# Kernel tuning notes

Measured on AMD Instinct MI355X. Metric: run time of the kernel, lower is better.

## Reference

```python
import jax, jax.numpy as jnp
import numpy as np

B, C_LIDAR, C_CAM = 2, 384, 80
H = W = 180
HW = H * W
HID, NCLS, P, NH, DFF, L, NMS_K = 128, 10, 200, 8, 256, 2, 3


def conv2d(x, w, b):
    y = jax.lax.conv_general_dilated(x, w, (1, 1), 'SAME', dimension_numbers=('NCHW', 'OIHW', 'NCHW'))
    return y + b[None, :, None, None]


def conv1d3(x, w, b):
    y = jax.lax.conv_general_dilated(x, w, (1,), 'SAME', dimension_numbers=('NCH', 'OIH', 'NCH'))
    return y + b[None, :, None]


def layer_norm(x, g, b, eps=1e-5):
    mu = jnp.mean(x, -1, keepdims=True)
    var = jnp.mean((x - mu) ** 2, -1, keepdims=True)
    return (x - mu) * jax.lax.rsqrt(var + eps) * g + b


def mha(q, k, v, wqkv, bqkv, wo, bo):
    Bq, Nq, C = q.shape
    dh = C // NH
    qh = (q @ wqkv[0].T + bqkv[0]).reshape(Bq, Nq, NH, dh)
    kh = (k @ wqkv[1].T + bqkv[1]).reshape(k.shape[0], -1, NH, dh)
    vh = (v @ wqkv[2].T + bqkv[2]).reshape(v.shape[0], -1, NH, dh)
    att = jax.nn.softmax(jnp.einsum('bqhd,bkhd->bhqk', qh, kh) * np.float32(1.0 / np.sqrt(dh)), axis=-1)
    out = jnp.einsum('bhqk,bkhd->bqhd', att, vh).reshape(Bq, Nq, C)
    return out @ wo.T + bo


def posembed(pos, w1, b1, g, bt, w2, b2):
    # Conv1d(2->C,k1) + BN(inference) + ReLU + Conv1d(C->C,k1); pos [B,N,2] -> [B,N,C]
    x = pos @ w1.T + b1
    x = jax.nn.relu(x * g + bt)
    return x @ w2.T + b2


def reference(lidar, cam, shared_w, shared_b, fused_w, fused_b, hm_w1, hm_b1, hm_g, hm_beta, hm_w2, hm_b2, ce_w, ce_b, pe_w1, pe_b1, pe_g, pe_beta, pe_w2, pe_b2, attn_wqkv, attn_bqkv, attn_wo, attn_bo, ln_g, ln_b, ffn_w1, ffn_b1, ffn_w2, ffn_b2, hc_w1, hc_b1, hc_g, hc_beta, hc_w2, hc_b2, hh_w1, hh_b1, hh_g, hh_beta, hh_w2, hh_b2):
    cam_feat = conv2d(cam, fused_w, fused_b)            # [B,HID,H,W]
    lidar_feat = conv2d(lidar, shared_w, shared_b)      # [B,HID,H,W]
    lidar_flat = lidar_feat.reshape(B, HID, HW)
    key_flat = cam_feat.reshape(B, HID, HW).transpose(0, 2, 1)   # [B,HW,HID]
    # heatmap head: ConvModule(conv+BN+ReLU) then conv -> classes
    h = jax.nn.relu(conv2d(lidar_feat, hm_w1, hm_b1) * hm_g[None, :, None, None] + hm_beta[None, :, None, None])
    dense_heatmap = conv2d(h, hm_w2, hm_b2)             # [B,NCLS,H,W]
    heatmap = jax.nn.sigmoid(jax.lax.stop_gradient(dense_heatmap))
    # max-pool local-max NMS
    pad = NMS_K // 2
    inner = jax.lax.reduce_window(heatmap, -jnp.inf, jax.lax.max, (1, 1, NMS_K, NMS_K), (1, 1, 1, 1), 'VALID')
    local_max = jnp.zeros_like(heatmap).at[:, :, pad:-pad, pad:-pad].set(inner)
    # nuScenes: classes 8,9 use kernel-size-1 pooling (identity)
    local_max = local_max.at[:, 8].set(heatmap[:, 8]).at[:, 9].set(heatmap[:, 9])
    heatmap = heatmap * (heatmap == local_max)
    # top-k proposals over flattened class*HW scores (== descending argsort[:P])
    _, top = jax.lax.top_k(heatmap.reshape(B, -1), P)
    top_cls = top // HW
    top_idx = top % HW
    qf = jnp.take_along_axis(lidar_flat, top_idx[:, None, :], axis=2)   # [B,HID,P]
    one_hot = jax.nn.one_hot(top_cls, NCLS, dtype=qf.dtype)             # [B,P,NCLS]
    qf = qf + (one_hot @ ce_w.T + ce_b).transpose(0, 2, 1)
    # BEV position grid (x/y cell centers, ij order matching HW flattening)
    gx = jnp.arange(H, dtype=qf.dtype) + 0.5
    gy = jnp.arange(W, dtype=qf.dtype) + 0.5
    bev = jnp.stack(jnp.meshgrid(gx, gy, indexing='ij'), -1).reshape(HW, 2)
    qpos = bev[top_idx]                                  # [B,P,2]
    x = qf.transpose(0, 2, 1)                            # [B,P,HID]
    for i in range(L):
        qpe = posembed(qpos, pe_w1[i, 0], pe_b1[i, 0], pe_g[i, 0], pe_beta[i, 0], pe_w2[i, 0], pe_b2[i, 0])
        kpe = posembed(bev[None], pe_w1[i, 1], pe_b1[i, 1], pe_g[i, 1], pe_beta[i, 1], pe_w2[i, 1], pe_b2[i, 1])
        k = key_flat + kpe
        sa = mha(x + qpe, x + qpe, x + qpe, attn_wqkv[i, 0], attn_bqkv[i, 0], attn_wo[i, 0], attn_bo[i, 0])
        x = layer_norm(x + sa, ln_g[i, 0], ln_b[i, 0])
        ca = mha(x + qpe, k, k, attn_wqkv[i, 1], attn_bqkv[i, 1], attn_wo[i, 1], attn_bo[i, 1])
        x = layer_norm(x + ca, ln_g[i, 1], ln_b[i, 1])
        f = jax.nn.relu(x @ ffn_w1[i].T + ffn_b1[i]) @ ffn_w2[i].T + ffn_b2[i]
        x = layer_norm(x + f, ln_g[i, 2], ln_b[i, 2])
        xc = x.transpose(0, 2, 1)                        # [B,HID,P]
        yc = jax.nn.relu(conv1d3(xc, hc_w1[i], hc_b1[i]) * hc_g[i][None, :, None] + hc_beta[i][None, :, None])
        center = conv1d3(yc, hc_w2[i], hc_b2[i]) + qpos.transpose(0, 2, 1)
        yh = jax.nn.relu(conv1d3(xc, hh_w1[i], hh_b1[i]) * hh_g[i][None, :, None] + hh_beta[i][None, :, None])
        hm_pred = conv1d3(yh, hh_w2[i], hh_b2[i])
        qpos = jax.lax.stop_gradient(center).transpose(0, 2, 1)   # .detach().clone().permute
    return jnp.concatenate([center, hm_pred], axis=1)   # [B, 2+NCLS, P]


def _n(key, i, shape, s=0.02):
    return s * jax.random.normal(jax.random.fold_in(key, i), shape, dtype=jnp.float32)


def setup_inputs():
    key = jax.random.key(0)
    z, o = jnp.zeros, jnp.ones
    return dict(
        lidar=jax.random.normal(jax.random.fold_in(key, 100), (B, C_LIDAR, H, W), dtype=jnp.float32),
        cam=jax.random.normal(jax.random.fold_in(key, 101), (B, C_CAM, H, W), dtype=jnp.float32),
        shared_w=_n(key, 0, (HID, C_LIDAR, 3, 3)), shared_b=z((HID,)),
        fused_w=_n(key, 1, (HID, C_CAM, 3, 3)), fused_b=z((HID,)),
        hm_w1=_n(key, 2, (HID, HID, 3, 3)), hm_b1=z((HID,)), hm_g=o((HID,)), hm_beta=z((HID,)),
        hm_w2=_n(key, 3, (NCLS, HID, 3, 3)), hm_b2=z((NCLS,)),
        ce_w=_n(key, 4, (HID, NCLS)), ce_b=z((HID,)),
        pe_w1=_n(key, 5, (L, 2, HID, 2), 0.1), pe_b1=z((L, 2, HID)),
        pe_g=o((L, 2, HID)), pe_beta=z((L, 2, HID)),
        pe_w2=_n(key, 6, (L, 2, HID, HID)), pe_b2=z((L, 2, HID)),
        attn_wqkv=_n(key, 7, (L, 2, 3, HID, HID), 0.05), attn_bqkv=z((L, 2, 3, HID)),
        attn_wo=_n(key, 8, (L, 2, HID, HID), 0.05), attn_bo=z((L, 2, HID)),
        ln_g=o((L, 3, HID)), ln_b=z((L, 3, HID)),
        ffn_w1=_n(key, 9, (L, DFF, HID)), ffn_b1=z((L, DFF)),
        ffn_w2=_n(key, 10, (L, HID, DFF)), ffn_b2=z((L, HID)),
        hc_w1=_n(key, 11, (L, HID, HID, 3)), hc_b1=z((L, HID)), hc_g=o((L, HID)), hc_beta=z((L, HID)),
        hc_w2=_n(key, 12, (L, 2, HID, 3)), hc_b2=z((L, 2)),
        hh_w1=_n(key, 13, (L, HID, HID, 3)), hh_b1=z((L, HID)), hh_g=o((L, HID)), hh_beta=z((L, HID)),
        hh_w2=_n(key, 14, (L, NCLS, HID, 3)), hh_b2=z((L, NCLS)),
    )
```

## Files before the change

### kernel.cpp

```cpp
#include <hip/hip_runtime.h>
#include <hip/hip_bf16.h>

typedef __hip_bfloat16 bf16;
typedef _Float16 f16;

#define HW 32400
#define NCLS 10
#define PQ 200
#define HIDDEN 128
#define NSPLIT 45
#define SPLITLEN 720
#define CHK 32
#define CAP 6144
#define NBIN 4096
#define L2E 1.44269504f

typedef __attribute__((ext_vector_type(8))) _Float16 half8;
typedef __attribute__((ext_vector_type(8))) short short8;
typedef __attribute__((ext_vector_type(4))) short short4v;
typedef __attribute__((ext_vector_type(4))) float f32x4;

__device__ __forceinline__ float b2f(bf16 v) { return __bfloat162float(v); }
__device__ __forceinline__ void stf(float* p, float v) { *p = v; }
__device__ __forceinline__ void stf(bf16* p, float v) { *p = __float2bfloat16(v); }
__device__ __forceinline__ float ldsel(const void* p, long i, unsigned isbf) {
  return isbf ? __bfloat162float(((const bf16*)p)[i]) : ((const float*)p)[i];
}
__device__ __forceinline__ float ldf(const float* p, long i) { return p[i]; }
__device__ __forceinline__ float ldf(const bf16* p, long i) { return __bfloat162float(p[i]); }
__device__ __forceinline__ short f2bf_bits(float v) {
  union { bf16 h; short s; } u; u.h = __float2bfloat16(v); return u.s;
}
__device__ __forceinline__ short f2h_bits(float v) {
  union { f16 h; short s; } u; u.h = (f16)v; return u.s;
}

__global__ void detect_k(const unsigned* __restrict__ L, unsigned* __restrict__ FLAGS)
{
  __shared__ unsigned cnt[2];
  int tid = threadIdx.x;
  if (tid < 2) cnt[tid] = 0;
  __syncthreads();
  unsigned nz = 0, pl = 0;
  for (int w = tid; w < 4096; w += 256) {
    unsigned u = L[w];
    if (u) {
      nz++;
      unsigned e = (u >> 7) & 0xFF;
      if (e >= 110 && e <= 140) pl++;
    }
  }
  atomicAdd(&cnt[0], nz);
  atomicAdd(&cnt[1], pl);
  __syncthreads();
  if (tid == 0) {
    FLAGS[0] = (2u * cnt[1] > cnt[0]) ? 1u : 0u;
    FLAGS[1] = 0u;
  }
}

struct CvtArgs { const void* src[40]; int n[40]; int off[40]; };
__global__ __launch_bounds__(256) void cvt_k(CvtArgs a, float* __restrict__ dst,
                                             const unsigned* __restrict__ FLAGS)
{
  int j = blockIdx.y;
  unsigned isbf = FLAGS[0];
  int n = a.n[j];
  const void* s = a.src[j];
  float* d = dst + a.off[j];
  for (int t = blockIdx.x * 256 + threadIdx.x; t < n; t += gridDim.x * 256)
    d[t] = ldsel(s, t, isbf);
}

__global__ __launch_bounds__(256) void wprep_k(const float* __restrict__ Wsrc,
    short* __restrict__ WB, int N, int K, int KB, int NTG, int split,
    const unsigned* __restrict__ FLAGS, int dynmode)
{
  unsigned isbf = dynmode ? FLAGS[0] : 0u;
  long total = (long)(split ? 2 : 1) * 9 * KB * NTG * 512;
  for (long t = (long)blockIdx.x * 256 + threadIdx.x; t < total;
       t += (long)gridDim.x * 256) {
    long r = t;
    int k = (int)(r & 31); r >>= 5;
    int n16 = (int)(r & 15); r >>= 4;
    int nt = (int)(r % NTG); r /= NTG;
    int kb = (int)(r % KB); r /= KB;
    int tap = (int)(r % 9); r /= 9;
    int plane = (int)r;
    int n = nt * 16 + n16, kk = kb * 32 + k;
    float v = 0.f;
    if (n < N && kk < K) v = Wsrc[((long)n * K + kk) * 9 + tap];
    short outv;
    if (isbf) {
      outv = (plane == 0) ? f2bf_bits(v) : (short)0;
    } else {
      f16 h = (f16)v;
      if (plane == 0) outv = f2h_bits((float)h);
      else outv = f2h_bits((v - (float)h) * 4096.0f);
    }
    WB[t] = outv;
  }
}

template <int MODE, int WM, int WN, int MT, int NT, int CW, typename CT>
__global__ __launch_bounds__(256) void conv_mfma(
    const void* __restrict__ A, const unsigned* __restrict__ FLAGS, int dyn,
    int gate, long abatch,
    const short* __restrict__ WB, const float* __restrict__ bias,
    const float* __restrict__ g, const float* __restrict__ beta, int act,
    CT* __restrict__ C, long cbatch, int N, int K, int KB, int NTG)
{
  constexpr int CPR = 180 / CW;
  constexpr int TOT = 180 * CPR;
  constexpr int BAND = (TOT + 7) / 8;
  constexpr int PXS = WM * MT * 16 + 2;
  constexpr int AW = 3 * PXS * 40;
  __shared__ __align__(16) short Ah[AW];
  __shared__ __align__(16) short Al[MODE == 3 ? AW : 8];
  if (gate >= 0 && FLAGS[0] != (unsigned)gate) return;
  int gsw = blockIdx.x;
  int idx = (gsw & 7) * BAND + (gsw >> 3);
  if (idx >= TOT) return;
  unsigned isbf = dyn ? FLAGS[0] : 0u;
  int bz = blockIdx.z;
  int y = idx / CPR;
  int x0 = (idx % CPR) * CW;
  int tid = threadIdx.x;
  int w = tid >> 6, lane = tid & 63;
  int lane15 = lane & 15, lgrp = lane >> 4;
  int wm = w % WM, wn = w / WM;
  int mbase = wm * MT * 16;
  int nbase = wn * NT * 16;
  f32x4 accM[MT][NT] = {};
  f32x4 accC[MODE == 3 ? MT : 1][MODE == 3 ? NT : 1] = {};
  long planeStride = (long)9 * KB * NTG * 512;

  for (int kb = 0; kb < KB; kb++) {
    __syncthreads();
    for (int u = tid; u < 3 * PXS * 4; u += 256) {
      int px = u % PXS;
      int t2 = u / PXS;
      int kg = t2 & 3, row = t2 >> 2;
      int gx = x0 + px - 1, gy = y + row - 1;
      bool in = (gx >= 0 && gx < 180 && gy >= 0 && gy < 180);
      long gbase = (long)bz * abatch + (long)(kb * 32 + kg * 8) * HW +
                   (long)gy * 180 + gx;
      short8 hv, lv;
#pragma unroll
      for (int j = 0; j < 8; j++) {
        int kk = kb * 32 + kg * 8 + j;
        if constexpr (MODE == 1) {
          hv[j] = (in && kk < K) ? ((const short*)A)[gbase + (long)j * HW]
                                 : (short)0;
        } else {
          float v = (in && kk < K) ? ldsel(A, gbase + (long)j * HW, isbf) : 0.f;
          f16 h = (f16)v;
          hv[j] = f2h_bits((float)h);
          if constexpr (MODE == 3) lv[j] = f2h_bits((v - (float)h) * 4096.0f);
        }
      }
      int o = (row * PXS + px) * 40 + kg * 8;
      *(short8*)&Ah[o] = hv;
      if constexpr (MODE == 3) *(short8*)&Al[o] = lv;
    }
    __syncthreads();
#pragma unroll
    for (int tap = 0; tap < 9; tap++) {
      int ty = tap / 3, tx = tap % 3;
      const short* wb = WB + (((long)tap * KB + kb) * NTG) * 512;
      if constexpr (MODE == 1) {
        short8 bh[NT];
#pragma unroll
        for (int nt = 0; nt < NT; nt++) {
          long o = (long)(wn * NT + nt) * 512 + lane15 * 32 + lgrp * 8;
          bh[nt] = *(const short8*)(wb + o);
        }
        short8 ah[MT];
#pragma unroll
        for (int mt = 0; mt < MT; mt++) {
          int px = mbase + mt * 16 + lane15 + tx;
          ah[mt] = *(const short8*)&Ah[(ty * PXS + px) * 40 + lgrp * 8];
        }
#pragma unroll
        for (int mt = 0; mt < MT; mt++)
#pragma unroll
          for (int nt = 0; nt < NT; nt++)
            accM[mt][nt] = __builtin_amdgcn_mfma_f32_16x16x32_bf16(
                ah[mt], bh[nt], accM[mt][nt], 0, 0, 0);
      } else {
        half8 bh[NT], bl[MODE == 3 ? NT : 1];
#pragma unroll
        for (int nt = 0; nt < NT; nt++) {
          long o = (long)(wn * NT + nt) * 512 + lane15 * 32 + lgrp * 8;
          bh[nt] = *(const half8*)(wb + o);
          if constexpr (MODE == 3) bl[nt] = *(const half8*)(wb + planeStride + o);
        }
        half8 ah[MT], al[MODE == 3 ? MT : 1];
#pragma unroll
        for (int mt = 0; mt < MT; mt++) {
          int px = mbase + mt * 16 + lane15 + tx;
          int o = (ty * PXS + px) * 40 + lgrp * 8;
          ah[mt] = *(const half8*)&Ah[o];
          if constexpr (MODE == 3) al[mt] = *(const half8*)&Al[o];
        }
#pragma unroll
        for (int mt = 0; mt < MT; mt++)
#pragma unroll
          for (int nt = 0; nt < NT; nt++) {
            accM[mt][nt] = __builtin_amdgcn_mfma_f32_16x16x32_f16(
                ah[mt], bh[nt], accM[mt][nt], 0, 0, 0);
            if constexpr (MODE == 3) {
              accC[mt][nt] = __builtin_amdgcn_mfma_f32_16x16x32_f16(
                  al[mt], bh[nt], accC[mt][nt], 0, 0, 0);
              accC[mt][nt] = __builtin_amdgcn_mfma_f32_16x16x32_f16(
                  ah[mt], bl[nt], accC[mt][nt], 0, 0, 0);
            }
          }
      }
    }
  }
  int pixbase = y * 180 + x0;
#pragma unroll
  for (int mt = 0; mt < MT; mt++) {
    int m = mbase + mt * 16 + lgrp * 4;
    if (m >= CW) continue;
#pragma unroll
    for (int nt = 0; nt < NT; nt++) {
      int n = nbase + nt * 16 + lane15;
      if (n >= N) continue;
      float bi = bias[n];
      float gg = g ? g[n] : 1.f;
      float bb = g ? beta[n] : 0.f;
      long base = (long)bz * cbatch + (long)n * HW + pixbase + m;
      float vv[4];
#pragma unroll
      for (int r = 0; r < 4; r++) {
        float v = accM[mt][nt][r];
        if constexpr (MODE == 3) v += accC[mt][nt][r] * (1.f / 4096.f);
        v += bi;
        if (g) v = v * gg + bb;
        if (act == 1) v = fmaxf(v, 0.f);
        else if (act == 2) v = 1.f / (1.f + expf(-v));
        vv[r] = v;
      }
      if constexpr (sizeof(CT) == 4) {
        if (m + 3 < CW) {
          f32x4 ov; ov[0] = vv[0]; ov[1] = vv[1]; ov[2] = vv[2]; ov[3] = vv[3];
          *(f32x4*)&C[base] = ov;
        } else {
#pragma unroll
          for (int r = 0; r < 4; r++) if (m + r < CW) C[base + r] = vv[r];
        }
      } else {
        if (m + 3 < CW) {
          short4v ov;
#pragma unroll
          for (int r = 0; r < 4; r++) ov[r] = f2bf_bits(vv[r]);
          *(short4v*)&C[base] = ov;
        } else {
#pragma unroll
          for (int r = 0; r < 4; r++)
            if (m + r < CW) *((short*)&C[base + r]) = f2bf_bits(vv[r]);
        }
      }
    }
  }
}

__global__ __launch_bounds__(256) void kvproj_k(
    const bf16* __restrict__ A1, const bf16* __restrict__ A2,
    const float* __restrict__ Wf, const float* __restrict__ bias,
    bf16* __restrict__ C)
{
  __shared__ __align__(16) short As[64 * 40];
  int m0 = blockIdx.x * 64;
  int n0 = blockIdx.y * 64;
  int b = blockIdx.z;
  int tid = threadIdx.x;
  int w = tid >> 6, lane = tid & 63;
  int lane15 = lane & 15, lgrp = lane >> 4;
  int wm = w & 1, wn = w >> 1;
  const bf16* A1b = A1 + (long)b * 128 * HW;
  f32x4 acc[2][2] = {};
  for (int kb = 0; kb < 4; kb++) {
    __syncthreads();
    for (int e = tid; e < 2048; e += 256) {
      int k = e >> 6, m = e & 63;
      int gm = m0 + m;
      float v = 0.f;
      if (gm < HW) {
        long idx = (long)(kb * 32 + k) * HW + gm;
        v = b2f(A1b[idx]) + b2f(A2[idx]);
      }
      As[m * 40 + k] = f2bf_bits(v);
    }
    __syncthreads();
    short8 bh[2];
#pragma unroll
    for (int nt = 0; nt < 2; nt++) {
      int n = n0 + wn * 32 + nt * 16 + lane15;
      const float* wr = Wf + (long)n * 128 + kb * 32 + lgrp * 8;
      float4 w0 = *(const float4*)wr;
      float4 w1 = *(const float4*)(wr + 4);
      short8 t;
      t[0] = f2bf_bits(w0.x); t[1] = f2bf_bits(w0.y);
      t[2] = f2bf_bits(w0.z); t[3] = f2bf_bits(w0.w);
      t[4] = f2bf_bits(w1.x); t[5] = f2bf_bits(w1.y);
      t[6] = f2bf_bits(w1.z); t[7] = f2bf_bits(w1.w);
      bh[nt] = t;
    }
    short8 ah[2];
#pragma unroll
    for (int mt = 0; mt < 2; mt++) {
      int m = wm * 32 + mt * 16 + lane15;
      ah[mt] = *(const short8*)&As[m * 40 + lgrp * 8];
    }
#pragma unroll
    for (int mt = 0; mt < 2; mt++)
#pragma unroll
      for (int nt = 0; nt < 2; nt++)
        acc[mt][nt] = __builtin_amdgcn_mfma_f32_16x16x32_bf16(
            ah[mt], bh[nt], acc[mt][nt], 0, 0, 0);
  }
#pragma unroll
  for (int mt = 0; mt < 2; mt++) {
    int mq = m0 + wm * 32 + mt * 16 + lgrp * 4;
    if (mq >= HW) continue;
#pragma unroll
    for (int nt = 0; nt < 2; nt++) {
      int n = n0 + wn * 32 + nt * 16 + lane15;
      float bi = bias[n];
      short4v ov;
#pragma unroll
      for (int r = 0; r < 4; r++) ov[r] = f2bf_bits(acc[mt][nt][r] + bi);
      *(short4v*)&C[(long)b * 256 * HW + (long)n * HW + mq] = ov;
    }
  }
}

__global__ __launch_bounds__(256) void kpe_mfma_k(
    const float* __restrict__ pe1w, const float* __restrict__ pe1b,
    const float* __restrict__ pe1g, const float* __restrict__ pe1bt,
    const float* __restrict__ W2, const float* __restrict__ b2,
    bf16* __restrict__ C)
{
  __shared__ __align__(16) short As[64 * 40];
  int m0 = blockIdx.x * 64;
  int n0 = blockIdx.y * 64;
  int tid = threadIdx.x;
  int w = tid >> 6, lane = tid & 63;
  int lane15 = lane & 15, lgrp = lane >> 4;
  int wm = w & 1, wn = w >> 1;
  f32x4 acc[2][2] = {};
  for (int kb = 0; kb < 4; kb++) {
    __syncthreads();
    for (int e = tid; e < 2048; e += 256) {
      int k = e >> 6, m = e & 63;
      int gm = m0 + m;
      int kk = kb * 32 + k;
      float v = 0.f;
      if (gm < HW) {
        float p0 = (float)(gm / 180) + 0.5f;
        float p1 = (float)(gm % 180) + 0.5f;
        float t = p0 * pe1w[kk * 2] + p1 * pe1w[kk * 2 + 1] + pe1b[kk];
        t = t * pe1g[kk] + pe1bt[kk];
        v = fmaxf(t, 0.f);
      }
      As[m * 40 + k] = f2bf_bits(v);
    }
    __syncthreads();
    short8 bh[2];
#pragma unroll
    for (int nt = 0; nt < 2; nt++) {
      int n = n0 + wn * 32 + nt * 16 + lane15;
      const float* wr = W2 + (long)n * 128 + kb * 32 + lgrp * 8;
      float4 w0 = *(const float4*)wr;
      float4 w1 = *(const float4*)(wr + 4);
      short8 t;
      t[0] = f2bf_bits(w0.x); t[1] = f2bf_bits(w0.y);
      t[2] = f2bf_bits(w0.z); t[3] = f2bf_bits(w0.w);
      t[4] = f2bf_bits(w1.x); t[5] = f2bf_bits(w1.y);
      t[6] = f2bf_bits(w1.z); t[7] = f2bf_bits(w1.w);
      bh[nt] = t;
    }
    short8 ah[2];
#pragma unroll
    for (int mt = 0; mt < 2; mt++) {
      int m = wm * 32 + mt * 16 + lane15;
      ah[mt] = *(const short8*)&As[m * 40 + lgrp * 8];
    }
#pragma unroll
    for (int mt = 0; mt < 2; mt++)
#pragma unroll
      for (int nt = 0; nt < 2; nt++)
        acc[mt][nt] = __builtin_amdgcn_mfma_f32_16x16x32_bf16(
            ah[mt], bh[nt], acc[mt][nt], 0, 0, 0);
  }
#pragma unroll
  for (int mt = 0; mt < 2; mt++) {
    int mq = m0 + wm * 32 + mt * 16 + lgrp * 4;
    if (mq >= HW) continue;
#pragma unroll
    for (int nt = 0; nt < 2; nt++) {
      int n = n0 + wn * 32 + nt * 16 + lane15;
      float bi = b2[n];
      short4v ov;
#pragma unroll
      for (int r = 0; r < 4; r++) ov[r] = f2bf_bits(acc[mt][nt][r] + bi);
      *(short4v*)&C[(long)n * HW + mq] = ov;
    }
  }
}

template <typename AT, typename CT>
__global__ __launch_bounds__(256) void gemm_k(
    const AT* __restrict__ A, const AT* __restrict__ A2, int lda, int amode,
    long abatch,
    const float* __restrict__ W, const float* __restrict__ bias, int act,
    const float* __restrict__ res,
    const float* __restrict__ pe1w, const float* __restrict__ pe1b,
    const float* __restrict__ pe1g, const float* __restrict__ pe1bt,
    CT* __restrict__ C, int ldc, int cmode, long cbatch,
    int M, int N, int K)
{
  __shared__ __align__(16) float As[16][68];
  __shared__ __align__(16) float Ws[16][68];
  int b = blockIdx.z;
  int m0 = blockIdx.x * 64, n0 = blockIdx.y * 64;
  int tid = threadIdx.x;
  int nt = tid & 15, mt = tid >> 4;
  float acc[4][4] = {};
  const AT* Ab = A + (long)b * abatch;
  for (int k0 = 0; k0 < K; k0 += 16) {
    if (amode == 0) {
      for (int e = tid; e < 1024; e += 256) {
        int m = e >> 4, k = e & 15;
        float v = 0.f;
        if (m0 + m < M) {
          long idx = (long)(m0 + m) * lda + k0 + k;
          v = ldf(Ab, idx);
          if (A2) v += ldf(A2, idx);
        }
        As[k][m] = v;
      }
    } else {
      const float* qp = (const float*)A;
      for (int e = tid; e < 1024; e += 256) {
        int m = e & 63, k = e >> 6;
        float v = 0.f;
        int gm = m0 + m;
        if (gm < M) {
          float p0 = qp[gm * 2], p1 = qp[gm * 2 + 1];
          int kk = k0 + k;
          float t = p0 * pe1w[kk * 2] + p1 * pe1w[kk * 2 + 1] + pe1b[kk];
          t = t * pe1g[kk] + pe1bt[kk];
          v = fmaxf(t, 0.f);
        }
        As[k][m] = v;
      }
    }
    for (int e = tid; e < 1024; e += 256) {
      int n = e >> 4, k = e & 15;
      float v = 0.f;
      if (n0 + n < N) v = W[(long)(n0 + n) * K + k0 + k];
      Ws[k][n] = v;
    }
    __syncthreads();
#pragma unroll
    for (int kk = 0; kk < 16; kk++) {
      float4 av = *(const float4*)&As[kk][mt * 4];
      float4 wv = *(const float4*)&Ws[kk][nt * 4];
      float am[4] = {av.x, av.y, av.z, av.w};
      float wn[4] = {wv.x, wv.y, wv.z, wv.w};
#pragma unroll
      for (int mi = 0; mi < 4; mi++)
#pragma unroll
        for (int ni = 0; ni < 4; ni++)
          acc[mi][ni] = fmaf(am[mi], wn[ni], acc[mi][ni]);
    }
    __syncthreads();
  }
#pragma unroll
  for (int mi = 0; mi < 4; mi++) {
    int m = m0 + mt * 4 + mi;
    if (m >= M) continue;
#pragma unroll
    for (int ni = 0; ni < 4; ni++) {
      int n = n0 + nt * 4 + ni;
      if (n >= N) continue;
      float v = acc[mi][ni];
      if (bias) v += bias[n];
      if (act == 1) v = fmaxf(v, 0.f);
      if (res) v += res[(long)m * ldc + n];
      long ci = (cmode == 0) ? ((long)b * cbatch + (long)m * ldc + n)
                             : ((long)b * cbatch + (long)n * ldc + m);
      stf(&C[ci], v);
    }
  }
}

__global__ void nms_k(const float* __restrict__ HEAT, float* __restrict__ SCORE)
{
  int t = blockIdx.x * 256 + threadIdx.x;
  if (t >= 2 * NCLS * HW) return;
  int b = t / (NCLS * HW); int r = t % (NCLS * HW);
  int cls = r / HW; int n = r % HW;
  const float* hb = HEAT + ((long)(b * NCLS + cls)) * HW;
  float v = hb[n];
  bool keep = true;
  if (cls < 8) {
    int y = n / 180, x = n % 180;
    if (y == 0 || y == 179 || x == 0 || x == 179) keep = false;
    else {
      float mx = -1e30f;
#pragma unroll
      for (int dy = -1; dy <= 1; dy++)
#pragma unroll
        for (int dx = -1; dx <= 1; dx++)
          mx = fmaxf(mx, hb[(y + dy) * 180 + x + dx]);
      keep = (v == mx);
    }
  }
  SCORE[(long)b * (NCLS * HW) + r] = keep ? v : 0.f;
}

__global__ void zero_u32(unsigned* p, int n)
{
  int t = blockIdx.x * 256 + threadIdx.x;
  if (t < n) p[t] = 0;
}

__global__ __launch_bounds__(256) void hist_k(const float* __restrict__ SCORE,
                                              unsigned* __restrict__ HIST)
{
  __shared__ unsigned lh[NBIN];
  int b = blockIdx.y;
  for (int e = threadIdx.x; e < NBIN; e += 256) lh[e] = 0;
  __syncthreads();
  int start = blockIdx.x * 1350;
  const float* sb = SCORE + (long)b * (NCLS * HW);
  for (int e = start + threadIdx.x; e < start + 1350; e += 256) {
    unsigned bits = __float_as_uint(sb[e]);
    atomicAdd(&lh[bits >> 18], 1u);
  }
  __syncthreads();
  for (int e = threadIdx.x; e < NBIN; e += 256) {
    unsigned c = lh[e];
    if (c) atomicAdd(&HIST[b * NBIN + e], c);
  }
}

__global__ void thresh_k(const unsigned* __restrict__ HIST, unsigned* __restrict__ THR)
{
  __shared__ unsigned ps[256];
  int b = blockIdx.x;
  const unsigned* hb = HIST + b * NBIN;
  unsigned s = 0;
  for (int j = 0; j < 16; j++) s += hb[threadIdx.x * 16 + j];
  ps[threadIdx.x] = s;
  __syncthreads();
  if (threadIdx.x == 0) {
    unsigned cum = 0; int t = 255;
    for (; t > 0; t--) { if (cum + ps[t] >= PQ) break; cum += ps[t]; }
    int bin = t * 16 + 15;
    for (; bin > t * 16; bin--) { unsigned c = hb[bin]; if (cum + c >= PQ) break; cum += c; }
    if (bin < 1) bin = 1;
    THR[b] = (unsigned)bin;
  }
}

__global__ void collect_k(const float* __restrict__ SCORE, const unsigned* __restrict__ THR,
                          unsigned* __restrict__ ACNT, unsigned long long* __restrict__ CAND)
{
  int t = blockIdx.x * 256 + threadIdx.x;
  if (t >= 2 * NCLS * HW) return;
  int b = t / (NCLS * HW); int r = t % (NCLS * HW);
  float v = SCORE[(long)b * (NCLS * HW) + r];
  unsigned bits = __float_as_uint(v);
  if ((bits >> 18) >= THR[b]) {
    unsigned slot = atomicAdd(&ACNT[b], 1u);
    if (slot < CAP) CAND[(long)b * CAP + slot] =
        ((unsigned long long)bits << 32) | (unsigned)(~r);
  }
}

__global__ __launch_bounds__(64) void select_k(
    const unsigned long long* __restrict__ CAND, const unsigned* __restrict__ ACNT,
    unsigned* __restrict__ TOPC, unsigned* __restrict__ TOPI, float* __restrict__ QPA)
{
  __shared__ unsigned long long cnd[CAP];
  int b = blockIdx.x;
  int lane = threadIdx.x;
  unsigned cnt = ACNT[b]; if (cnt > CAP) cnt = CAP;
  for (int e = lane; e < (int)cnt; e += 64) cnd[e] = CAND[(long)b * CAP + e];
  __syncthreads();
  for (int p = 0; p < PQ; p++) {
    unsigned long long best = 0;
    for (int e = lane; e < (int)cnt; e += 64) { unsigned long long c = cnd[e]; if (c > best) best = c; }
#pragma unroll
    for (int o = 32; o; o >>= 1) {
      unsigned long long other = __shfl_xor(best, o, 64);
      if (other > best) best = other;
    }
    for (int e = lane; e < (int)cnt; e += 64) if (best != 0 && cnd[e] == best) cnd[e] = 0;
    if (lane == 0) {
      unsigned idx = (best == 0) ? 0u : ~(unsigned)(best & 0xFFFFFFFFull);
      if (idx >= NCLS * HW) idx = 0;
      unsigned cls = idx / HW, n = idx % HW;
      TOPC[b * PQ + p] = cls; TOPI[b * PQ + p] = n;
      QPA[((long)(b * PQ + p)) * 2 + 0] = (float)(n / 180) + 0.5f;
      QPA[((long)(b * PQ + p)) * 2 + 1] = (float)(n % 180) + 0.5f;
    }
    __syncthreads();
  }
}

__global__ void gather_k(const float* __restrict__ LIDF, const unsigned* __restrict__ TOPC,
                         const unsigned* __restrict__ TOPI, const float* __restrict__ cew,
                         const float* __restrict__ ceb, float* __restrict__ X)
{
  int t = blockIdx.x * 256 + threadIdx.x;
  if (t >= 2 * PQ * HIDDEN) return;
  int c = t & 127; int r = t >> 7; int p = r % PQ; int b = r / PQ;
  unsigned n = TOPI[b * PQ + p]; unsigned cls = TOPC[b * PQ + p];
  if (n >= HW) n = 0;
  if (cls >= NCLS) cls = 0;
  X[t] = LIDF[((long)(b * HIDDEN + c)) * HW + n] + cew[c * NCLS + cls] + ceb[c];
}

__global__ __launch_bounds__(64) void self_attn_k(const float* __restrict__ SQKV,
                                                  float* __restrict__ SAO)
{
  int q = blockIdx.x, h = blockIdx.y, b = blockIdx.z;
  int lane = threadIdx.x;
  const float* qp = SQKV + ((long)(b * PQ + q)) * 384 + h * 16;
  float qv[16];
#pragma unroll
  for (int d = 0; d < 16; d++) qv[d] = qp[d] * 0.25f;
  float sv[4]; int kks[4]; int nk = 0;
  float lmax = -1e30f;
  for (int kk = lane; kk < PQ; kk += 64) {
    const float* kp = SQKV + ((long)(b * PQ + kk)) * 384 + 128 + h * 16;
    float s = 0.f;
#pragma unroll
    for (int d = 0; d < 16; d++) s = fmaf(qv[d], kp[d], s);
    sv[nk] = s; kks[nk] = kk; nk++;
    lmax = fmaxf(lmax, s);
  }
#pragma unroll
  for (int o = 32; o; o >>= 1) lmax = fmaxf(lmax, __shfl_xor(lmax, o, 64));
  float lsum = 0.f; float acc[16] = {};
  for (int t = 0; t < nk; t++) {
    float p = expf(sv[t] - lmax);
    lsum += p;
    const float* vp = SQKV + ((long)(b * PQ + kks[t])) * 384 + 256 + h * 16;
#pragma unroll
    for (int d = 0; d < 16; d++) acc[d] = fmaf(p, vp[d], acc[d]);
  }
#pragma unroll
  for (int o = 32; o; o >>= 1) lsum += __shfl_xor(lsum, o, 64);
#pragma unroll
  for (int d = 0; d < 16; d++) {
    float v = acc[d];
#pragma unroll
    for (int o = 32; o; o >>= 1) v += __shfl_xor(v, o, 64);
    if (lane == 0) SAO[((long)(b * PQ + q)) * HIDDEN + h * 16 + d] = v / lsum;
  }
}

__global__ __launch_bounds__(256) void flash_mfma_k(const float* __restrict__ QH,
                                                    const bf16* __restrict__ KVT,
                                                    float* __restrict__ PART)
{
  __shared__ __align__(16) short Qs[64 * 40];
  __shared__ __align__(16) short Ks[2][32 * 40];
  __shared__ __align__(16) short Vs[2][16 * 40];
  __shared__ __align__(16) short Ps[4][16 * 40];
  int s = blockIdx.x, h = blockIdx.y;
  int b = blockIdx.z >> 2, qb = blockIdx.z & 3;
  int tid = threadIdx.x;
  int w = tid >> 6, lane = tid & 63;
  int lane15 = lane & 15, lgrp = lane >> 4;
  const short* Kb = (const short*)KVT + ((long)b * 256 + h * 16) * HW;
  const short* Vb = Kb + (long)128 * HW;
  int nbeg = s * SPLITLEN;

  for (int e = tid; e < 2 * 32 * 16; e += 256) {
    int buf = e >> 9, rr = e & 511;
    int kk = rr >> 4, d2 = rr & 15;
    Ks[buf][kk * 40 + 16 + d2] = 0;
  }
  {
    int q = tid >> 2, dg = tid & 3;
    int gq = qb * 64 + q;
    short8 v = {};
    if (dg < 2 && gq < PQ) {
      const float* qp = QH + ((long)(b * PQ + gq)) * HIDDEN + h * 16 + dg * 8;
#pragma unroll
      for (int j = 0; j < 8; j++) v[j] = f2bf_bits(qp[j] * 0.25f);
    }
    *(short8*)&Qs[q * 40 + dg * 8] = v;
  }

  auto stageKV = [&](int t, int buf) {
    int kb0 = nbeg + t * CHK;
    for (int e = tid; e < 512; e += 256) {
      int d = e >> 5, kk = e & 31;
      long gk = kb0 + kk; if (gk >= HW) gk = HW - 1;
      long go = (long)d * HW + gk;
      Ks[buf][kk * 40 + d] = Kb[go];
      Vs[buf][d * 40 + kk] = Vb[go];
    }
  };

  stageKV(0, 0);
  __syncthreads();

  short8 aq = *(const short8*)&Qs[(w * 16 + lane15) * 40 + lgrp * 8];
  float m[4] = {-1e30f, -1e30f, -1e30f, -1e30f};
  float l[4] = {0.f, 0.f, 0.f, 0.f};
  f32x4 accO = {};
  const int NTL = (SPLITLEN + CHK - 1) / CHK;
  for (int t = 0; t < NTL; t++) {
    int cur = t & 1;
    if (t + 1 < NTL) stageKV(t + 1, cur ^ 1);
    int valid = SPLITLEN - t * CHK; if (valid > CHK) valid = CHK;
    short8 bk0 = *(const short8*)&Ks[cur][lane15 * 40 + lgrp * 8];
    short8 bk1 = *(const short8*)&Ks[cur][(16 + lane15) * 40 + lgrp * 8];
    f32x4 z = {};
    f32x4 s0 = __builtin_amdgcn_mfma_f32_16x16x32_bf16(aq, bk0, z, 0, 0, 0);
    f32x4 s1 = __builtin_amdgcn_mfma_f32_16x16x32_bf16(aq, bk1, z, 0, 0, 0);
    bool msk0 = (lane15 >= valid);
    bool msk1 = (16 + lane15 >= valid);
#pragma unroll
    for (int r = 0; r < 4; r++) {
      float x0 = msk0 ? -1e30f : s0[r];
      float x1 = msk1 ? -1e30f : s1[r];
      float mx = fmaxf(x0, x1);
      mx = fmaxf(mx, __shfl_xor(mx, 1, 64));
      mx = fmaxf(mx, __shfl_xor(mx, 2, 64));
      mx = fmaxf(mx, __shfl_xor(mx, 4, 64));
      mx = fmaxf(mx, __shfl_xor(mx, 8, 64));
      float mn = fmaxf(m[r], mx);
      float p0 = exp2f((x0 - mn) * L2E);
      float p1 = exp2f((x1 - mn) * L2E);
      float sum = p0 + p1;
      sum += __shfl_xor(sum, 1, 64);
      sum += __shfl_xor(sum, 2, 64);
      sum += __shfl_xor(sum, 4, 64);
      sum += __shfl_xor(sum, 8, 64);
      float al = exp2f((m[r] - mn) * L2E);
      l[r] = l[r] * al + sum;
      m[r] = mn;
      accO[r] *= al;
      Ps[w][(lgrp * 4 + r) * 40 + lane15] = f2bf_bits(p0);
      Ps[w][(lgrp * 4 + r) * 40 + 16 + lane15] = f2bf_bits(p1);
    }
    short8 ap = *(const short8*)&Ps[w][lane15 * 40 + lgrp * 8];
    short8 bv = *(const short8*)&Vs[cur][lane15 * 40 + lgrp * 8];
    accO = __builtin_amdgcn_mfma_f32_16x16x32_bf16(ap, bv, accO, 0, 0, 0);
    __syncthreads();
  }
  long base = ((((long)(b * 8 + h)) * NSPLIT + s) * PQ) * 18;
#pragma unroll
  for (int r = 0; r < 4; r++) {
    int gq = qb * 64 + w * 16 + lgrp * 4 + r;
    if (gq < PQ) {
      long ro = base + (long)gq * 18;
      PART[ro + lane15] = accO[r];
      if (lane15 == 0) { PART[ro + 16] = m[r]; PART[ro + 17] = l[r]; }
    }
  }
}

__global__ void combine_k(const float* __restrict__ PART, float* __restrict__ CAO)
{
  int t = blockIdx.x * 256 + threadIdx.x;
  if (t >= 2 * 8 * PQ * 16) return;
  int d = t & 15; int r = t >> 4;
  int q = r % PQ; r /= PQ;
  int h = r & 7; int b = r >> 3;
  long base = (((long)(b * 8 + h)) * NSPLIT) * PQ * 18 + (long)q * 18;
  float M = -1e30f;
  for (int s = 0; s < NSPLIT; s++) M = fmaxf(M, PART[base + (long)s * PQ * 18 + 16]);
  float L = 0.f, O = 0.f;
  for (int s = 0; s < NSPLIT; s++) {
    long p0 = base + (long)s * PQ * 18;
    float w = expf(PART[p0 + 16] - M);
    L += PART[p0 + 17] * w;
    O += PART[p0 + d] * w;
  }
  CAO[((long)(b * PQ + q)) * HIDDEN + h * 16 + d] = (L > 0.f) ? O / L : 0.f;
}

__global__ __launch_bounds__(256) void ln_k(const float* __restrict__ PRE,
                                            const float* __restrict__ g,
                                            const float* __restrict__ bta,
                                            float* __restrict__ X)
{
  int row = blockIdx.x * 4 + (threadIdx.x >> 6);
  int lane = threadIdx.x & 63;
  const float* p = PRE + (long)row * HIDDEN;
  float v0 = p[lane], v1 = p[lane + 64];
  float s = v0 + v1;
#pragma unroll
  for (int o = 32; o; o >>= 1) s += __shfl_xor(s, o, 64);
  float mu = s * (1.f / 128.f);
  float d0 = v0 - mu, d1 = v1 - mu;
  float vs = d0 * d0 + d1 * d1;
#pragma unroll
  for (int o = 32; o; o >>= 1) vs += __shfl_xor(vs, o, 64);
  float rs = rsqrtf(vs * (1.f / 128.f) + 1e-5f);
  float* xo = X + (long)row * HIDDEN;
  xo[lane] = d0 * rs * g[lane] + bta[lane];
  xo[lane + 64] = d1 * rs * g[lane + 64] + bta[lane + 64];
}

__global__ __launch_bounds__(128) void conv1d_k(const float* __restrict__ X,
                                                const float* __restrict__ w,
                                                const float* __restrict__ bias,
                                                const float* __restrict__ g,
                                                const float* __restrict__ beta,
                                                float* __restrict__ Y)
{
  int p = blockIdx.x, b = blockIdx.y;
  int co = threadIdx.x;
  __shared__ float xs[3][HIDDEN];
  for (int e = co; e < 3 * HIDDEN; e += HIDDEN) {
    int t = e >> 7, c = e & 127;
    int pp = p + t - 1;
    xs[t][c] = (pp >= 0 && pp < PQ) ? X[((long)(b * PQ + pp)) * HIDDEN + c] : 0.f;
  }
  __syncthreads();
  const float* wr = w + (long)co * HIDDEN * 3;
  float acc = 0.f;
  for (int c = 0; c < HIDDEN; c++) {
    acc = fmaf(xs[0][c], wr[c * 3 + 0], acc);
    acc = fmaf(xs[1][c], wr[c * 3 + 1], acc);
    acc = fmaf(xs[2][c], wr[c * 3 + 2], acc);
  }
  float v = (acc + bias[co]) * g[co] + beta[co];
  Y[((long)(b * PQ + p)) * HIDDEN + co] = fmaxf(v, 0.f);
}

__global__ void head2_k(const float* __restrict__ Y, const float* __restrict__ w,
                        const float* __restrict__ bias, const float* __restrict__ qpos,
                        float* __restrict__ OUT, int N, float* __restrict__ qnext)
{
  int t = blockIdx.x * 256 + threadIdx.x;
  if (t >= 2 * N * PQ) return;
  int p = t % PQ; int r = t / PQ; int co = r % N; int b = r / N;
  const float* wr = w + (long)co * HIDDEN * 3;
  float acc = 0.f;
  for (int tap = 0; tap < 3; tap++) {
    int pp = p + tap - 1;
    if (pp < 0 || pp >= PQ) continue;
    const float* yr = Y + ((long)(b * PQ + pp)) * HIDDEN;
    for (int c = 0; c < HIDDEN; c++)
      acc = fmaf(yr[c], wr[c * 3 + tap], acc);
  }
  float v = acc + bias[co];
  if (qpos) v += qpos[((long)(b * PQ + p)) * 2 + co];
  OUT[((long)(b * N + co)) * PQ + p] = v;
  if (qnext) qnext[((long)(b * PQ + p)) * 2 + co] = v;
}

__global__ void out_k(const float* __restrict__ CENT, const float* __restrict__ HMP,
                      void* __restrict__ out, const unsigned* __restrict__ FLAGS)
{
  int t = blockIdx.x * 256 + threadIdx.x;
  if (t >= 2 * 12 * PQ) return;
  int p = t % PQ; int r = t / PQ; int ch = r % 12; int b = r / 12;
  float v = (ch < 2) ? CENT[((long)(b * 2 + ch)) * PQ + p]
                     : HMP[((long)(b * 10 + ch - 2)) * PQ + p];
  if (FLAGS[0]) ((bf16*)out)[t] = __float2bfloat16(v);
  else          ((float*)out)[t] = v;
}

extern "C" void kernel_launch(void* const* d_in, const int* in_sizes, int n_in,
                              void* d_out, int out_size, void* d_ws, size_t ws_size,
                              hipStream_t stream)
{
  (void)n_in; (void)out_size;

  float* F = (float*)d_ws;
  size_t off = 0;
  int aoff[42];
  {
    size_t acc = 0;
    for (int i = 2; i < 42; i++) { aoff[i] = (int)acc; acc += (size_t)in_sizes[i]; }
    off = acc;
  }
  float* ARENA = F;
  float* LIDF = F + off;
  bf16*  KVT16 = (bf16*)(F + off);
  off += 8294400;
  float* HBUF = F + off;
  bf16*  KPET16 = (bf16*)(F + off);
  float* PART  = F + off;
  off += 4147200;
  bf16*  CAMF16 = (bf16*)(F + off);
  off += 4147200;
  float* HEAT  = F + off;
  float* SCORE = F + off + 648000;
  off += 1296000;
  float* X   = F + off; off += 51200;
  float* XQ  = F + off; off += 51200;
  float* QPE = F + off; off += 51200;
  float* T1Q = F + off; off += 51200;
  float* SQKV = F + off; off += 153600;
  float* SAO = F + off; off += 51200;
  float* PRE = F + off; off += 51200;
  float* QH2 = F + off; off += 51200;
  float* CAO = F + off; off += 51200;
  float* FF1 = F + off; off += 102400;
  float* YC  = F + off; off += 51200;
  float* CENT = F + off; off += 800;
  float* HMP = F + off; off += 4000;
  float* QPA = F + off; off += 800;
  float* QPB = F + off; off += 800;
  unsigned* U = (unsigned*)(F + off);
  unsigned* HIST  = U;
  unsigned* ACNT  = U + 8192;
  unsigned* THR   = U + 8194;
  unsigned* FLAGS = U + 8196;
  unsigned* TOPC  = U + 8198;
  unsigned* TOPI  = U + 8598;
  unsigned long long* CAND = (unsigned long long*)(U + 9000);
  size_t end_floats = off + 9000 + 2 * CAP * 2;
  float* HBUF2 = nullptr;
  if (ws_size >= (end_floats + 8294400) * sizeof(float))
    HBUF2 = F + end_floats;
  short* WB_LID = (short*)((((uintptr_t)X) + 15) & ~(uintptr_t)15);
  short* WB_CAM = WB_LID + 884736;
  short* WB_HM1 = WB_CAM + 110592;
  short* WB_HM2 = WB_HM1 + 294912;

  auto W = [&](int i) -> const float* { return ARENA + aoff[i]; };

  detect_k<<<1, 256, 0, stream>>>((const unsigned*)d_in[0], FLAGS);
  {
    CvtArgs a;
    for (int i = 2; i < 42; i++) { a.src[i - 2] = d_in[i]; a.n[i - 2] = in_sizes[i]; a.off[i - 2] = aoff[i]; }
    cvt_k<<<dim3(432, 40), 256, 0, stream>>>(a, ARENA, FLAGS);
  }
  wprep_k<<<3456, 256, 0, stream>>>(W(2), WB_LID, 128, 384, 12, 8, 1, FLAGS, 1);
  wprep_k<<<432, 256, 0, stream>>>(W(4), WB_CAM, 128, 80, 3, 8, 0, FLAGS, 1);
  wprep_k<<<1152, 256, 0, stream>>>(W(6), WB_HM1, 128, 128, 4, 8, 1, FLAGS, 0);
  wprep_k<<<144, 256, 0, stream>>>(W(10), WB_HM2, 10, 128, 4, 1, 1, FLAGS, 0);

  auto gemm = [&](const float* A, const float* A2, int lda, const float* Wp,
                  const float* bias, int act, const float* res, float* C, int ldc,
                  int M, int N, int K) {
    dim3 grid((M + 63) / 64, (N + 63) / 64, 1);
    gemm_k<float, float><<<grid, 256, 0, stream>>>(
        A, A2, lda, 0, 0L, Wp, bias, act, res,
        nullptr, nullptr, nullptr, nullptr, C, ldc, 0, 0L, M, N, K);
  };

  conv_mfma<1, 1, 4, 4, 2, 60, float><<<dim3(544, 1, 2), 256, 0, stream>>>(
      d_in[0], FLAGS, 1, 1, (long)384 * HW, WB_LID, W(3), nullptr, nullptr, 0,
      LIDF, (long)128 * HW, 128, 384, 12, 8);
  conv_mfma<3, 1, 4, 4, 2, 60, float><<<dim3(544, 1, 2), 256, 0, stream>>>(
      d_in[0], FLAGS, 1, 0, (long)384 * HW, WB_LID, W(3), nullptr, nullptr, 0,
      LIDF, (long)128 * HW, 128, 384, 12, 8);
  conv_mfma<1, 1, 4, 4, 2, 60, bf16><<<dim3(544, 1, 2), 256, 0, stream>>>(
      d_in[1], FLAGS, 1, 1, (long)80 * HW, WB_CAM, W(5), nullptr, nullptr, 0,
      CAMF16, (long)128 * HW, 128, 80, 3, 8);
  conv_mfma<0, 1, 4, 4, 2, 60, bf16><<<dim3(544, 1, 2), 256, 0, stream>>>(
      d_in[1], FLAGS, 1, 0, (long)80 * HW, WB_CAM, W(5), nullptr, nullptr, 0,
      CAMF16, (long)128 * HW, 128, 80, 3, 8);
  if (HBUF2) {
    conv_mfma<3, 1, 4, 4, 2, 60, float><<<dim3(544, 1, 2), 256, 0, stream>>>(
        LIDF, FLAGS, 0, -1, (long)128 * HW, WB_HM1, W(7), W(8), W(9), 1,
        HBUF2, (long)128 * HW, 128, 128, 4, 8);
    conv_mfma<3, 4, 1, 1, 1, 60, float><<<dim3(544, 1, 2), 256, 0, stream>>>(
        HBUF2, FLAGS, 0, -1, (long)128 * HW, WB_HM2, W(11), nullptr, nullptr, 2,
        HEAT, (long)NCLS * HW, 10, 128, 4, 1);
  } else {
    for (int b = 0; b < 2; b++) {
      conv_mfma<3, 1, 4, 4, 2, 60, float><<<dim3(544, 1, 1), 256, 0, stream>>>(
          LIDF + (long)b * 128 * HW, FLAGS, 0, -1, 0L, WB_HM1, W(7), W(8), W(9), 1,
          HBUF, 0L, 128, 128, 4, 8);
      conv_mfma<3, 4, 1, 1, 1, 60, float><<<dim3(544, 1, 1), 256, 0, stream>>>(
          HBUF, FLAGS, 0, -1, 0L, WB_HM2, W(11), nullptr, nullptr, 2,
          HEAT + (long)b * NCLS * HW, 0L, 10, 128, 4, 1);
    }
  }

  nms_k<<<(2 * NCLS * HW + 255) / 256, 256, 0, stream>>>(HEAT, SCORE);
  zero_u32<<<(8196 + 255) / 256, 256, 0, stream>>>(U, 8196);
  hist_k<<<dim3(240, 2), 256, 0, stream>>>(SCORE, HIST);
  thresh_k<<<2, 256, 0, stream>>>(HIST, THR);
  collect_k<<<(2 * NCLS * HW + 255) / 256, 256, 0, stream>>>(SCORE, THR, ACNT, CAND);
  select_k<<<2, 64, 0, stream>>>(CAND, ACNT, TOPC, TOPI, QPA);
  gather_k<<<200, 256, 0, stream>>>(LIDF, TOPC, TOPI, W(12), W(13), X);

  for (int i = 0; i < 2; i++) {
    const float* qcur = (i == 0) ? QPA : QPB;
    float* qnext = (i == 0) ? QPB : QPA;
    gemm_k<float, float><<<dim3(7, 2, 1), 256, 0, stream>>>(
        qcur, (const float*)nullptr, 0, 3, 0L,
        W(18) + (size_t)(i * 2 + 0) * 16384, W(19) + (i * 2 + 0) * 128, 0, nullptr,
        W(14) + (i * 2 + 0) * 256, W(15) + (i * 2 + 0) * 128,
        W(16) + (i * 2 + 0) * 128, W(17) + (i * 2 + 0) * 128,
        QPE, 128, 0, 0L, 400, 128, 128);
    kpe_mfma_k<<<dim3(507, 2), 256, 0, stream>>>(
        W(14) + (i * 2 + 1) * 256, W(15) + (i * 2 + 1) * 128,
        W(16) + (i * 2 + 1) * 128, W(17) + (i * 2 + 1) * 128,
        W(18) + (size_t)(i * 2 + 1) * 16384, W(19) + (i * 2 + 1) * 128,
        KPET16);
    gemm(X, QPE, 128, W(20) + (size_t)(i * 2 + 0) * 49152, W(21) + (i * 2 + 0) * 384,
         0, nullptr, SQKV, 384, 400, 384, 128);
    self_attn_k<<<dim3(200, 8, 2), 64, 0, stream>>>(SQKV, SAO);
    gemm(SAO, nullptr, 128, W(22) + (size_t)(i * 2 + 0) * 16384, W(23) + (i * 2 + 0) * 128,
         0, X, PRE, 128, 400, 128, 128);
    ln_k<<<100, 256, 0, stream>>>(PRE, W(24) + (i * 3 + 0) * 128, W(25) + (i * 3 + 0) * 128, X);
    gemm(X, QPE, 128, W(20) + (size_t)(i * 2 + 1) * 49152, W(21) + (i * 2 + 1) * 384,
         0, nullptr, QH2, 128, 400, 128, 128);
    kvproj_k<<<dim3(507, 4, 2), 256, 0, stream>>>(
        CAMF16, KPET16,
        W(20) + (size_t)(i * 2 + 1) * 49152 + 16384,
        W(21) + (i * 2 + 1) * 384 + 128, KVT16);
    flash_mfma_k<<<dim3(NSPLIT, 8, 8), 256, 0, stream>>>(QH2, KVT16, PART);
    combine_k<<<200, 256, 0, stream>>>(PART, CAO);
    gemm(CAO, nullptr, 128, W(22) + (size_t)(i * 2 + 1) * 16384, W(23) + (i * 2 + 1) * 128,
         0, X, PRE, 128, 400, 128, 128);
    ln_k<<<100, 256, 0, stream>>>(PRE, W(24) + (i * 3 + 1) * 128, W(25) + (i * 3 + 1) * 128, X);
    gemm(X, nullptr, 128, W(26) + (size_t)i * 32768, W(27) + i * 256,
         1, nullptr, FF1, 256, 400, 256, 128);
    gemm(FF1, nullptr, 256, W(28) + (size_t)i * 32768, W(29) + i * 128,
         0, X, PRE, 128, 400, 128, 256);
    ln_k<<<100, 256, 0, stream>>>(PRE, W(24) + (i * 3 + 2) * 128, W(25) + (i * 3 + 2) * 128, X);
    conv1d_k<<<dim3(200, 2), 128, 0, stream>>>(X, W(30) + (size_t)i * 49152,
        W(31) + i * 128, W(32) + i * 128, W(33) + i * 128, YC);
    head2_k<<<4, 256, 0, stream>>>(YC, W(34) + (size_t)i * 768, W(35) + i * 2,
        qcur, CENT, 2, qnext);
    conv1d_k<<<dim3(200, 2), 128, 0, stream>>>(X, W(36) + (size_t)i * 49152,
        W(37) + i * 128, W(38) + i * 128, W(39) + i * 128, YC);
    head2_k<<<16, 256, 0, stream>>>(YC, W(40) + (size_t)i * 3840, W(41) + i * 10,
        nullptr, HMP, 10, nullptr);
  }
  out_k<<<19, 256, 0, stream>>>(CENT, HMP, d_out, FLAGS);
}
```

Baseline: 1.903 ms.

## Batch conv tile global loads before LDS stores; widen kvproj N-tile to 128

```diff
diff --git a/kernel.cpp b/kernel.cpp
--- a/kernel.cpp
+++ b/kernel.cpp
@@ -115,6 +115,8 @@
   constexpr int BAND = (TOT + 7) / 8;
   constexpr int PXS = WM * MT * 16 + 2;
   constexpr int AW = 3 * PXS * 40;
+  constexpr int UTOT = 3 * PXS * 4;
+  constexpr int NU = (UTOT + 255) / 256;
   __shared__ __align__(16) short Ah[AW];
   __shared__ __align__(16) short Al[MODE == 3 ? AW : 8];
   if (gate >= 0 && FLAGS[0] != (unsigned)gate) return;
@@ -137,31 +139,83 @@
 
   for (int kb = 0; kb < KB; kb++) {
     __syncthreads();
-    for (int u = tid; u < 3 * PXS * 4; u += 256) {
-      int px = u % PXS;
-      int t2 = u / PXS;
-      int kg = t2 & 3, row = t2 >> 2;
-      int gx = x0 + px - 1, gy = y + row - 1;
-      bool in = (gx >= 0 && gx < 180 && gy >= 0 && gy < 180);
-      long gbase = (long)bz * abatch + (long)(kb * 32 + kg * 8) * HW +
-                   (long)gy * 180 + gx;
-      short8 hv, lv;
-#pragma unroll
-      for (int j = 0; j < 8; j++) {
-        int kk = kb * 32 + kg * 8 + j;
-        if constexpr (MODE == 1) {
-          hv[j] = (in && kk < K) ? ((const short*)A)[gbase + (long)j * HW]
-                                 : (short)0;
-        } else {
-          float v = (in && kk < K) ? ldsel(A, gbase + (long)j * HW, isbf) : 0.f;
-          f16 h = (f16)v;
-          hv[j] = f2h_bits((float)h);
-          if constexpr (MODE == 3) lv[j] = f2h_bits((v - (float)h) * 4096.0f);
+    if constexpr (MODE == 1) {
+      short8 hv8[NU];
+#pragma unroll
+      for (int iu = 0; iu < NU; iu++) {
+        int u = tid + iu * 256;
+        if (u < UTOT) {
+          int px = u % PXS;
+          int t2 = u / PXS;
+          int kg = t2 & 3, row = t2 >> 2;
+          int gx = x0 + px - 1, gy = y + row - 1;
+          bool in = (gx >= 0 && gx < 180 && gy >= 0 && gy < 180);
+          long gbase = (long)bz * abatch + (long)(kb * 32 + kg * 8) * HW +
+                       (long)gy * 180 + gx;
+          short8 v = {};
+          if (in) {
+#pragma unroll
+            for (int j = 0; j < 8; j++) {
+              int kk = kb * 32 + kg * 8 + j;
+              v[j] = (kk < K) ? ((const short*)A)[gbase + (long)j * HW]
+                              : (short)0;
+            }
+          }
+          hv8[iu] = v;
         }
       }
-      int o = (row * PXS + px) * 40 + kg * 8;
-      *(short8*)&Ah[o] = hv;
-      if constexpr (MODE == 3) *(short8*)&Al[o] = lv;
+#pragma unroll
+      for (int iu = 0; iu < NU; iu++) {
+        int u = tid + iu * 256;
+        if (u < UTOT) {
+          int px = u % PXS;
+          int t2 = u / PXS;
+          int kg = t2 & 3, row = t2 >> 2;
+          int o = (row * PXS + px) * 40 + kg * 8;
+          *(short8*)&Ah[o] = hv8[iu];
+        }
+      }
+    } else {
+      float pv[NU][8];
+#pragma unroll
+      for (int iu = 0; iu < NU; iu++) {
+        int u = tid + iu * 256;
+        if (u < UTOT) {
+          int px = u % PXS;
+          int t2 = u / PXS;
+          int kg = t2 & 3, row = t2 >> 2;
+          int gx = x0 + px - 1, gy = y + row - 1;
+          bool in = (gx >= 0 && gx < 180 && gy >= 0 && gy < 180);
+          long gbase = (long)bz * abatch + (long)(kb * 32 + kg * 8) * HW +
+                       (long)gy * 180 + gx;
+#pragma unroll
+          for (int j = 0; j < 8; j++) {
+            int kk = kb * 32 + kg * 8 + j;
+            pv[iu][j] =
+                (in && kk < K) ? ldsel(A, gbase + (long)j * HW, isbf) : 0.f;
+          }
+        }
+      }
+#pragma unroll
+      for (int iu = 0; iu < NU; iu++) {
+        int u = tid + iu * 256;
+        if (u < UTOT) {
+          int px = u % PXS;
+          int t2 = u / PXS;
+          int kg = t2 & 3, row = t2 >> 2;
+          int o = (row * PXS + px) * 40 + kg * 8;
+          short8 hv, lv;
+#pragma unroll
+          for (int j = 0; j < 8; j++) {
+            float v = pv[iu][j];
+            f16 h = (f16)v;
+            hv[j] = f2h_bits((float)h);
+            if constexpr (MODE == 3) lv[j] = f2h_bits((v - (float)h) * 4096.0f);
+          }
+          *(short8*)&Ah[o] = hv;
+          if constexpr (MODE == 3) *(short8*)&Al[o] = lv;
+        }
+      }
     }
     __syncthreads();
 #pragma unroll
@@ -274,14 +328,14 @@
 {
   __shared__ __align__(16) short As[64 * 40];
   int m0 = blockIdx.x * 64;
-  int n0 = blockIdx.y * 64;
+  int n0 = blockIdx.y * 128;
   int b = blockIdx.z;
   int tid = threadIdx.x;
   int w = tid >> 6, lane = tid & 63;
   int lane15 = lane & 15, lgrp = lane >> 4;
   int wm = w & 1, wn = w >> 1;
   const bf16* A1b = A1 + (long)b * 128 * HW;
-  f32x4 acc[2][2] = {};
+  f32x4 acc[2][4] = {};
   for (int kb = 0; kb < 4; kb++) {
     __syncthreads();
     for (int e = tid; e < 2048; e += 256) {
@@ -295,10 +349,10 @@
       As[m * 40 + k] = f2bf_bits(v);
     }
     __syncthreads();
-    short8 bh[2];
-#pragma unroll
-    for (int nt = 0; nt < 2; nt++) {
-      int n = n0 + wn * 32 + nt * 16 + lane15;
+    short8 bh[4];
+#pragma unroll
+    for (int nt = 0; nt < 4; nt++) {
+      int n = n0 + wn * 64 + nt * 16 + lane15;
       const float* wr = Wf + (long)n * 128 + kb * 32 + lgrp * 8;
       float4 w0 = *(const float4*)wr;
       float4 w1 = *(const float4*)(wr + 4);
@@ -318,7 +372,7 @@
 #pragma unroll
     for (int mt = 0; mt < 2; mt++)
 #pragma unroll
-      for (int nt = 0; nt < 2; nt++)
+      for (int nt = 0; nt < 4; nt++)
         acc[mt][nt] = __builtin_amdgcn_mfma_f32_16x16x32_bf16(
             ah[mt], bh[nt], acc[mt][nt], 0, 0, 0);
   }
@@ -327,8 +381,8 @@
     int mq = m0 + wm * 32 + mt * 16 + lgrp * 4;
     if (mq >= HW) continue;
 #pragma unroll
-    for (int nt = 0; nt < 2; nt++) {
-      int n = n0 + wn * 32 + nt * 16 + lane15;
+    for (int nt = 0; nt < 4; nt++) {
+      int n = n0 + wn * 64 + nt * 16 + lane15;
       float bi = bias[n];
       short4v ov;
 #pragma unroll
@@ -1018,7 +1072,7 @@
     ln_k<<<100, 256, 0, stream>>>(PRE, W(24) + (i * 3 + 0) * 128, W(25) + (i * 3 + 0) * 128, X);
     gemm(X, QPE, 128, W(20) + (size_t)(i * 2 + 1) * 49152, W(21) + (i * 2 + 1) * 384,
          0, nullptr, QH2, 128, 400, 128, 128);
-    kvproj_k<<<dim3(507, 4, 2), 256, 0, stream>>>(
+    kvproj_k<<<dim3(507, 2, 2), 256, 0, stream>>>(
         CAMF16, KPET16,
         W(20) + (size_t)(i * 2 + 1) * 49152 + 16384,
         W(21) + (i * 2 + 1) * 384 + 128, KVT16);
```

Result: slower. 2.286 ms (+20.1%).
